# Optimization experiments

Measured on AMD Instinct MI355X. Metric: run time of the kernel, lower is better.

Reference implementation:

```python
import jax, jax.numpy as jnp
import numpy as np

B, L, N = 16, 512, 32          # batch, seq_length, feature_size
E = 128                        # embed_size == frequency_size (number_frequency=1)
EMB = 8                        # embedding_dim
FCH = 64                       # fc_hidden_dim
H = 256                        # hidden_size
PRE = 96                       # pre_length
LAMBDA = 0.01                  # sparsity_threshold
SCALE = 0.02                   # init_scale


def softshrink(v, lambd=LAMBDA):
    return jnp.where(v > lambd, v - lambd, jnp.where(v < -lambd, v + lambd, 0.0))


def setup_inputs() -> dict:
    key = jax.random.key(0)
    ks = jax.random.split(key, 16)
    f32 = jnp.float32
    return {
        "x": jax.random.normal(ks[0], (B, L, N), f32),
        "emb": jax.random.normal(ks[1], (1, E), f32),
        "w0": SCALE * jax.random.normal(ks[2], (2, E, E), f32),
        "b0": SCALE * jax.random.normal(ks[3], (2, E), f32),
        "w1": SCALE * jax.random.normal(ks[4], (2, E, E), f32),
        "b1": SCALE * jax.random.normal(ks[5], (2, E), f32),
        "w2": SCALE * jax.random.normal(ks[6], (2, E, E), f32),
        "b2": SCALE * jax.random.normal(ks[7], (2, E), f32),
        "emb10": jax.random.normal(ks[8], (L, EMB), f32),
        "fc1_w": jax.random.normal(ks[9], (FCH, E * EMB), f32) / np.sqrt(E * EMB),
        "fc1_b": jnp.zeros((FCH,), f32),
        "fc2_w": jax.random.normal(ks[10], (H, FCH), f32) / np.sqrt(FCH),
        "fc2_b": jnp.zeros((H,), f32),
        "fc3_w": jax.random.normal(ks[11], (PRE, H), f32) / np.sqrt(H),
        "fc3_b": jnp.zeros((PRE,), f32),
    }


def _diag(w):
    # einsum 'bli,ii->bli' multiplies by the DIAGONAL of w only
    return jnp.diagonal(w, axis1=-2, axis2=-1)


def reference(x, emb, w0, b0, w1, b1, w2, b2, emb10,
              fc1_w, fc1_b, fc2_w, fc2_b, fc3_w, fc3_b):
    Bb = x.shape[0]
    xt = jnp.transpose(x, (0, 2, 1)).reshape(Bb, -1)          # [B, N*L]
    tok = xt[:, :, None] * emb                                 # [B, N*L, E]
    xf = jnp.fft.rfft(tok, axis=1, norm="ortho")               # [B, N*L//2+1, E] complex
    bias = xf

    # --- fourierGC (faithful to the torch op ordering, incl. o_real reuse) ---
    relu = jax.nn.relu
    d00, d01 = _diag(w0[0]), _diag(w0[1])
    o_r = relu(xf.real * d00 - xf.imag * d01 + b0[0])
    o_i = relu(xf.imag * d00 + xf.real * d01 + b0[1])
    prev = softshrink(jnp.stack([o_r, o_i], axis=-1))

    # middle layer (num_layers=3 -> one): note o_i uses the UPDATED o_r, as in torch
    d10, d11 = _diag(w1[0]), _diag(w1[1])
    o_r_new = relu(o_r * d10 - o_i * d11 + b1[0])
    o_i = relu(o_i * d10 + o_r_new * d11 + b1[1])
    o_r = o_r_new
    prev = softshrink(jnp.stack([o_r, o_i], axis=-1)) + prev

    # last layer
    d20, d21 = _diag(w2[0]), _diag(w2[1])
    o_r_new = relu(o_r * d20 - o_i * d21 + b2[0])
    o_i = relu(o_i * d20 + o_r_new * d21 + b2[1])
    z = softshrink(jnp.stack([o_r_new, o_i], axis=-1)) + prev
    zc = jax.lax.complex(z[..., 0], z[..., 1])

    xf = zc + bias
    xt = jnp.fft.irfft(xf, n=N * L, axis=1, norm="ortho")      # [B, N*L, E]
    xt = xt.reshape(Bb, N, L, E)
    xt = jnp.transpose(xt, (0, 1, 3, 2))                        # [B, N, E, L]
    h = jnp.matmul(xt, emb10)                                   # [B, N, E, EMB]
    h = h.reshape(Bb, N, E * EMB)

    lrelu = lambda v: jax.nn.leaky_relu(v, 0.01)
    h = lrelu(h @ fc1_w.T + fc1_b)
    h = lrelu(h @ fc2_w.T + fc2_b)
    out = h @ fc3_w.T + fc3_b                                   # [B, N, PRE]
    return out[:, 0, :]                                         # target_idx = 0
```

## Files before the change

kernel.cpp:

```cpp
#include <hip/hip_runtime.h>
#include <math.h>

#define Bsz   16
#define Lseq  512
#define Nfeat 32
#define E     128
#define EMB   8
#define FCH   64
#define Hd    256
#define PRE   96
#define M     16384
#define MH    8193
#define LAMBDA 0.01f

#define OFF_G   0
#define OFF_CS  524288
#define OFF_P   655376

#define TWO_PI_M   3.83495196971410293e-4f
#define TWO_PI_128 4.90873852123405245e-2f

__global__ __launch_bounds__(256)
void k_prep(const float* __restrict__ x, const float* __restrict__ emb10,
            float* __restrict__ ws) {
  __shared__ float smem[Lseq * EMB];
  int bid = blockIdx.x, tid = threadIdx.x;
  if (bid < 257) {
    for (int i = tid; i < Lseq * EMB; i += 256) smem[i] = emb10[i];
    __syncthreads();
    int floc = tid >> 5, tl = tid & 31;
    #pragma unroll
    for (int ff = 0; ff < 4; ++ff) {
      int f = bid * 32 + ff * 8 + floc;
      if (f <= 8192) {
        float ca[EMB], sa[EMB];
        #pragma unroll
        for (int m = 0; m < EMB; ++m) { ca[m] = 0.f; sa[m] = 0.f; }
        #pragma unroll 4
        for (int i = 0; i < 16; ++i) {
          int t = tl + 32 * i;
          int k = (f * t) & (M - 1);
          float ss, cc;
          sincosf((float)k * TWO_PI_M, &ss, &cc);
          const float* er = smem + t * EMB;
          #pragma unroll
          for (int m = 0; m < EMB; ++m) {
            ca[m] = fmaf(cc, er[m], ca[m]);
            sa[m] = fmaf(ss, er[m], sa[m]);
          }
        }
        #pragma unroll
        for (int off = 16; off >= 1; off >>= 1) {
          #pragma unroll
          for (int m = 0; m < EMB; ++m) {
            ca[m] += __shfl_xor(ca[m], off, 64);
            sa[m] += __shfl_xor(sa[m], off, 64);
          }
        }
        if (tl == 0) {
          float wf = (f == 0 || f == 8192) ? (1.0f / 128.0f) : (2.0f / 128.0f);
          float* o = ws + OFF_CS + f * 16;
          #pragma unroll
          for (int m = 0; m < EMB; ++m) { o[m] = ca[m] * wf; o[8 + m] = sa[m] * wf; }
        }
      }
    }
  } else {
    int v = bid - 257;
    int b = v >> 6, t1base = (v & 63) << 1;
    int t1loc = tid >> 7, idx = tid & 127;
    {
      int t = (t1base + t1loc) + 128 * idx;
      int n = t >> 9, l = t & 511;
      smem[t1loc * 128 + idx] = x[b * (Lseq * Nfeat) + l * Nfeat + n];
    }
    __syncthreads();
    int f1 = idx, t1 = t1base + t1loc;
    float s1, c1; sincosf((float)f1 * TWO_PI_128, &s1, &c1);
    float c2 = c1 * c1 - s1 * s1, s2 = 2.f * s1 * c1;
    float cA = 1.f, sA = 0.f, cB = c1, sB = s1;
    float grA = 0.f, giA = 0.f, grB = 0.f, giB = 0.f;
    const float* xc = smem + t1loc * 128;
    #pragma unroll 8
    for (int t2 = 0; t2 < 128; t2 += 2) {
      float x0 = xc[t2], x1 = xc[t2 + 1];
      grA = fmaf(x0, cA, grA); giA = fmaf(x0, -sA, giA);
      grB = fmaf(x1, cB, grB); giB = fmaf(x1, -sB, giB);
      float cn = cA * c2 - sA * s2; sA = sA * c2 + cA * s2; cA = cn;
      cn = cB * c2 - sB * s2;       sB = sB * c2 + cB * s2; cB = cn;
    }
    float gr = grA + grB, gi = giA + giB;
    float sb, cb; sincosf((float)(f1 * t1) * TWO_PI_M, &sb, &cb);
    float grr = gr * cb + gi * sb;
    float gii = gi * cb - gr * sb;
    float* G = ws + OFF_G + ((b * 128 + f1) * 128 + t1) * 2;
    G[0] = grr;
    G[1] = gii;
  }
}

__global__ __launch_bounds__(256)
void k_gcf(const float* __restrict__ emb,
           const float* __restrict__ w0, const float* __restrict__ b0,
           const float* __restrict__ w1, const float* __restrict__ b1,
           const float* __restrict__ w2, const float* __restrict__ b2,
           float* __restrict__ ws) {
  int f1 = blockIdx.x, b = blockIdx.y, tid = threadIdx.x;
  int nf2 = (f1 == 0) ? 65 : 64;
  __shared__ float2 Gs[132];
  __shared__ float2 Xs[65];
  __shared__ float red[E * EMB];
  if (tid < 128)
    Gs[(tid >> 5) * 33 + (tid & 31)] =
        ((const float2*)(ws + OFF_G + (b * 128 + f1) * 256))[tid];
  __syncthreads();
  {
    int lane = tid & 63, w = tid >> 6;
    int q = lane >> 4, f2l = lane & 15;
    int f2 = w * 16 + f2l;
    int r = (f2 * q) & 3;
    float c = (r == 0) ? 1.f : (r == 2) ? -1.f : 0.f;
    float s = (r == 1) ? 1.f : (r == 3) ? -1.f : 0.f;
    float s1, c1; sincosf((float)f2 * TWO_PI_128, &s1, &c1);
    float xr = 0.f, xi = 0.f;
    const float2* g = Gs + q * 33;
    #pragma unroll 8
    for (int k = 0; k < 32; ++k) {
      float2 gv = g[k];
      xr = fmaf(gv.x, c, xr); xr = fmaf(gv.y, s, xr);
      xi = fmaf(gv.y, c, xi); xi = fmaf(-gv.x, s, xi);
      float cn = c * c1 - s * s1; s = s * c1 + c * s1; c = cn;
    }
    xr += __shfl_xor(xr, 16, 64); xi += __shfl_xor(xi, 16, 64);
    xr += __shfl_xor(xr, 32, 64); xi += __shfl_xor(xi, 32, 64);
    if (lane < 16) Xs[f2] = make_float2(xr, xi);
    if (f1 == 0 && tid < 32) {
      float er = 0.f, ei = 0.f;
      #pragma unroll
      for (int j = 0; j < 4; ++j) {
        int t1v = tid * 4 + j;
        float2 gv = Gs[(t1v >> 5) * 33 + (t1v & 31)];
        float sg = (j & 1) ? -1.f : 1.f;
        er = fmaf(gv.x, sg, er); ei = fmaf(gv.y, sg, ei);
      }
      #pragma unroll
      for (int off = 1; off <= 16; off <<= 1) {
        er += __shfl_xor(er, off, 64);
        ei += __shfl_xor(ei, off, 64);
      }
      if (tid == 0) Xs[64] = make_float2(er, ei);
    }
  }
  __syncthreads();
  int e = tid & 127, fh = tid >> 7;
  float se  = emb[e] * (1.0f / 128.0f);
  float d00 = w0[e * 129], d01 = w0[E * E + e * 129];
  float c00 = b0[e],       c01 = b0[E + e];
  float d10 = w1[e * 129], d11 = w1[E * E + e * 129];
  float c10 = b1[e],       c11 = b1[E + e];
  float d20 = w2[e * 129], d21 = w2[E * E + e * 129];
  float c20 = b2[e],       c21 = b2[E + e];
  float acc[EMB];
  #pragma unroll
  for (int m = 0; m < EMB; ++m) acc[m] = 0.f;
  const float* csbase = ws + OFF_CS + f1 * 16;

  for (int i = fh; i < nf2; i += 2) {
    int iu = __builtin_amdgcn_readfirstlane(i);
    const float* cs = csbase + (iu << 11);
    float2 X = Xs[i];
    float xr = X.x * se, xi = X.y * se;
    float or0 = fmaxf(fmaf(xr, d00, fmaf(-xi, d01, c00)), 0.f);
    float oi0 = fmaxf(fmaf(xi, d00, fmaf(xr, d01, c01)), 0.f);
    float pr = fmaxf(or0 - LAMBDA, 0.f), pi = fmaxf(oi0 - LAMBDA, 0.f);
    float or1 = fmaxf(fmaf(or0, d10, fmaf(-oi0, d11, c10)), 0.f);
    float oi1 = fmaxf(fmaf(oi0, d10, fmaf(or1, d11, c11)), 0.f);
    pr += fmaxf(or1 - LAMBDA, 0.f); pi += fmaxf(oi1 - LAMBDA, 0.f);
    float u2r = fmaf(or1, d20, fmaf(-oi1, d21, c20));
    float or2 = fmaxf(u2r, 0.f);
    float u2i = fmaf(oi1, d20, fmaf(or2, d21, c21));
    float zr = fmaxf(u2r - LAMBDA, 0.f) + pr;
    float zi = fmaxf(u2i - LAMBDA, 0.f) + pi;
    #pragma unroll
    for (int m = 0; m < EMB; ++m)
      acc[m] = fmaf(zr, cs[m], fmaf(-zi, cs[8 + m], acc[m]));
  }
  __syncthreads();
  if (fh == 1) {
    #pragma unroll
    for (int m = 0; m < EMB; ++m) red[e * EMB + m] = acc[m];
  }
  __syncthreads();
  if (fh == 0) {
    float* P = ws + OFF_P + (f1 * 16 + b) * (E * EMB) + e * EMB;
    #pragma unroll
    for (int m = 0; m < EMB; ++m) P[m] = acc[m] + red[e * EMB + m];
  }
}

__global__ __launch_bounds__(1024)
void k_fc(const float* __restrict__ x, const float* __restrict__ emb,
          const float* __restrict__ emb10,
          const float* __restrict__ fc1w, const float* __restrict__ fc1b,
          const float* __restrict__ fc2w, const float* __restrict__ fc2b,
          const float* __restrict__ fc3w, const float* __restrict__ fc3b,
          const float* __restrict__ ws, float* __restrict__ out) {
  int b = blockIdx.x;
  __shared__ float h0s[E * EMB];
  __shared__ float h1s[FCH];
  __shared__ float h2s[Hd];
  __shared__ float hxs[EMB];
  int tid = threadIdx.x;
  int lane = tid & 63, w = tid >> 6;
  {
    int m = lane & 7, g8 = lane >> 3;
    int gg = w * 8 + g8;
    float p = 0.f;
    #pragma unroll
    for (int l = gg; l < Lseq; l += 128)
      p = fmaf(x[b * (Lseq * Nfeat) + l * Nfeat], emb10[l * EMB + m], p);
    p += __shfl_xor(p, 8, 64);
    p += __shfl_xor(p, 16, 64);
    p += __shfl_xor(p, 32, 64);
    if (lane < 8) h2s[w * 8 + lane] = p;
  }
  const float* P = ws + OFF_P + b * (E * EMB) + tid;
  float a = 0.f;
  #pragma unroll 16
  for (int j = 0; j < 128; ++j) a += P[j * (16 * E * EMB)];
  __syncthreads();
  if (tid < 8) {
    float s = 0.f;
    #pragma unroll
    for (int wv = 0; wv < 16; ++wv) s += h2s[wv * 8 + tid];
    hxs[tid] = s;
  }
  __syncthreads();
  h0s[tid] = a + emb[tid >> 3] * hxs[tid & 7];
  __syncthreads();
  #pragma unroll
  for (int oo = 0; oo < 4; ++oo) {
    int o = oo * 16 + w;
    const float* wr = fc1w + o * (E * EMB);
    float acc = 0.f;
    #pragma unroll
    for (int j = 0; j < 16; ++j) acc = fmaf(h0s[lane + 64 * j], wr[lane + 64 * j], acc);
    #pragma unroll
    for (int off = 32; off >= 1; off >>= 1) acc += __shfl_xor(acc, off, 64);
    if (lane == 0) { float v = acc + fc1b[o]; h1s[o] = v > 0.f ? v : 0.01f * v; }
  }
  __syncthreads();
  #pragma unroll
  for (int oo = 0; oo < 16; ++oo) {
    int o = oo * 16 + w;
    float acc = h1s[lane] * fc2w[o * FCH + lane];
    #pragma unroll
    for (int off = 32; off >= 1; off >>= 1) acc += __shfl_xor(acc, off, 64);
    if (lane == 0) { float v = acc + fc2b[o]; h2s[o] = v > 0.f ? v : 0.01f * v; }
  }
  __syncthreads();
  #pragma unroll
  for (int oo = 0; oo < 6; ++oo) {
    int o = oo * 16 + w;
    const float* wr = fc3w + o * Hd;
    float acc = 0.f;
    #pragma unroll
    for (int j = 0; j < 4; ++j) acc = fmaf(h2s[lane + 64 * j], wr[lane + 64 * j], acc);
    #pragma unroll
    for (int off = 32; off >= 1; off >>= 1) acc += __shfl_xor(acc, off, 64);
    if (lane == 0) out[b * PRE + o] = acc + fc3b[o];
  }
}

extern "C" void kernel_launch(void* const* d_in, const int* in_sizes, int n_in,
                              void* d_out, int out_size, void* d_ws, size_t ws_size,
                              hipStream_t stream) {
  const float* x     = (const float*)d_in[0];
  const float* emb   = (const float*)d_in[1];
  const float* w0    = (const float*)d_in[2];
  const float* b0    = (const float*)d_in[3];
  const float* w1    = (const float*)d_in[4];
  const float* b1    = (const float*)d_in[5];
  const float* w2    = (const float*)d_in[6];
  const float* b2    = (const float*)d_in[7];
  const float* emb10 = (const float*)d_in[8];
  const float* fc1w  = (const float*)d_in[9];
  const float* fc1b  = (const float*)d_in[10];
  const float* fc2w  = (const float*)d_in[11];
  const float* fc2b  = (const float*)d_in[12];
  const float* fc3w  = (const float*)d_in[13];
  const float* fc3b  = (const float*)d_in[14];
  float* ws  = (float*)d_ws;
  float* out = (float*)d_out;

  k_prep<<<dim3(1281), 256, 0, stream>>>(x, emb10, ws);
  k_gcf<<<dim3(128, Bsz), 256, 0, stream>>>(emb, w0, b0, w1, b1, w2, b2, ws);
  k_fc<<<dim3(Bsz), 1024, 0, stream>>>(x, emb, emb10, fc1w, fc1b, fc2w, fc2b,
                                       fc3w, fc3b, ws, out);
}
```

Measured before the change: 153.4 us.

## Merge prep phases, use hardware sin/cos, and batch four f1 rows per gcf block

k_prep now runs both the twiddle-DFT and the cos/sin projection table in every block instead of splitting them across disjoint block ranges. Its sincosf calls become hardware revolution-based sin/cos, and the f=8192 table entry is computed separately. k_gcf handles four f1 rows per block, using a full 128-point inner DFT in place of shuffle-reduced partial sums, which quarters the partial-sum buffer that k_fc must reduce. The intent is fewer launched blocks, cheaper transcendentals and less reduction traffic, at the cost of some hardware sin/cos accuracy and longer per-thread loops.

```diff
diff --git a/kernel.cpp b/kernel.cpp
--- a/kernel.cpp
+++ b/kernel.cpp
@@ -17,142 +17,146 @@
 #define OFF_CS  524288
 #define OFF_P   655376
 
-#define TWO_PI_M   3.83495196971410293e-4f
-#define TWO_PI_128 4.90873852123405245e-2f
-
-__global__ __launch_bounds__(256)
+#define REV_M   6.103515625e-5f
+#define REV_128 7.8125e-3f
+
+__device__ __forceinline__ float sin_rev(float r) { return __builtin_amdgcn_sinf(r); }
+__device__ __forceinline__ float cos_rev(float r) { return __builtin_amdgcn_cosf(r); }
+
+__global__ __launch_bounds__(256, 4)
 void k_prep(const float* __restrict__ x, const float* __restrict__ emb10,
             float* __restrict__ ws) {
-  __shared__ float smem[Lseq * EMB];
+  __shared__ __align__(16) float sbuf[4160];
   int bid = blockIdx.x, tid = threadIdx.x;
-  if (bid < 257) {
-    for (int i = tid; i < Lseq * EMB; i += 256) smem[i] = emb10[i];
-    __syncthreads();
-    int floc = tid >> 5, tl = tid & 31;
-    #pragma unroll
-    for (int ff = 0; ff < 4; ++ff) {
-      int f = bid * 32 + ff * 8 + floc;
-      if (f <= 8192) {
-        float ca[EMB], sa[EMB];
-        #pragma unroll
-        for (int m = 0; m < EMB; ++m) { ca[m] = 0.f; sa[m] = 0.f; }
-        #pragma unroll 4
-        for (int i = 0; i < 16; ++i) {
-          int t = tl + 32 * i;
-          int k = (f * t) & (M - 1);
-          float ss, cc;
-          sincosf((float)k * TWO_PI_M, &ss, &cc);
-          const float* er = smem + t * EMB;
-          #pragma unroll
-          for (int m = 0; m < EMB; ++m) {
-            ca[m] = fmaf(cc, er[m], ca[m]);
-            sa[m] = fmaf(ss, er[m], sa[m]);
-          }
-        }
-        #pragma unroll
-        for (int off = 16; off >= 1; off >>= 1) {
-          #pragma unroll
-          for (int m = 0; m < EMB; ++m) {
-            ca[m] += __shfl_xor(ca[m], off, 64);
-            sa[m] += __shfl_xor(sa[m], off, 64);
-          }
-        }
-        if (tl == 0) {
-          float wf = (f == 0 || f == 8192) ? (1.0f / 128.0f) : (2.0f / 128.0f);
-          float* o = ws + OFF_CS + f * 16;
-          #pragma unroll
-          for (int m = 0; m < EMB; ++m) { o[m] = ca[m] * wf; o[8 + m] = sa[m] * wf; }
-        }
-      }
-    }
-  } else {
-    int v = bid - 257;
-    int b = v >> 6, t1base = (v & 63) << 1;
+  {
+    int b = bid >> 6, t1base = (bid & 63) << 1;
     int t1loc = tid >> 7, idx = tid & 127;
     {
       int t = (t1base + t1loc) + 128 * idx;
       int n = t >> 9, l = t & 511;
-      smem[t1loc * 128 + idx] = x[b * (Lseq * Nfeat) + l * Nfeat + n];
+      sbuf[t1loc * 128 + idx] = x[b * (Lseq * Nfeat) + l * Nfeat + n];
     }
     __syncthreads();
     int f1 = idx, t1 = t1base + t1loc;
-    float s1, c1; sincosf((float)f1 * TWO_PI_128, &s1, &c1);
+    float s1 = sin_rev((float)f1 * REV_128), c1 = cos_rev((float)f1 * REV_128);
     float c2 = c1 * c1 - s1 * s1, s2 = 2.f * s1 * c1;
     float cA = 1.f, sA = 0.f, cB = c1, sB = s1;
     float grA = 0.f, giA = 0.f, grB = 0.f, giB = 0.f;
-    const float* xc = smem + t1loc * 128;
+    const float2* xc2 = (const float2*)(sbuf + t1loc * 128);
     #pragma unroll 8
-    for (int t2 = 0; t2 < 128; t2 += 2) {
-      float x0 = xc[t2], x1 = xc[t2 + 1];
-      grA = fmaf(x0, cA, grA); giA = fmaf(x0, -sA, giA);
-      grB = fmaf(x1, cB, grB); giB = fmaf(x1, -sB, giB);
+    for (int h = 0; h < 64; ++h) {
+      float2 xv = xc2[h];
+      grA = fmaf(xv.x, cA, grA); giA = fmaf(xv.x, -sA, giA);
+      grB = fmaf(xv.y, cB, grB); giB = fmaf(xv.y, -sB, giB);
       float cn = cA * c2 - sA * s2; sA = sA * c2 + cA * s2; cA = cn;
       cn = cB * c2 - sB * s2;       sB = sB * c2 + cB * s2; cB = cn;
     }
     float gr = grA + grB, gi = giA + giB;
-    float sb, cb; sincosf((float)(f1 * t1) * TWO_PI_M, &sb, &cb);
+    float rv = (float)(f1 * t1) * REV_M;
+    float sb = sin_rev(rv), cb = cos_rev(rv);
     float grr = gr * cb + gi * sb;
     float gii = gi * cb - gr * sb;
     float* G = ws + OFF_G + ((b * 128 + f1) * 128 + t1) * 2;
-    G[0] = grr;
-    G[1] = gii;
+    G[0] = grr; G[1] = gii;
+  }
+  __syncthreads();
+  {
+    for (int j = tid; j < Lseq * EMB; j += 256) {
+      int t = j >> 3, m = j & 7;
+      sbuf[m * 512 + t] = emb10[j];
+    }
+    __syncthreads();
+    int floc = tid >> 5, tl = tid & 31;
+    int f = bid * 8 + floc;
+    float ca[EMB], sa[EMB];
+    #pragma unroll
+    for (int m = 0; m < EMB; ++m) { ca[m] = 0.f; sa[m] = 0.f; }
+    #pragma unroll 4
+    for (int it = 0; it < 16; ++it) {
+      int t = tl + 32 * it;
+      int k = (f * t) & (M - 1);
+      float rv = (float)k * REV_M;
+      float cc = cos_rev(rv), ss = sin_rev(rv);
+      #pragma unroll
+      for (int m = 0; m < EMB; ++m) {
+        float ev = sbuf[m * 512 + t];
+        ca[m] = fmaf(cc, ev, ca[m]);
+        sa[m] = fmaf(ss, ev, sa[m]);
+      }
+    }
+    #pragma unroll
+    for (int off = 16; off >= 1; off >>= 1) {
+      #pragma unroll
+      for (int m = 0; m < EMB; ++m) {
+        ca[m] += __shfl_xor(ca[m], off, 64);
+        sa[m] += __shfl_xor(sa[m], off, 64);
+      }
+    }
+    if (tl == 0) {
+      float wf = (f == 0) ? (1.0f / 128.0f) : (2.0f / 128.0f);
+      float* o = ws + OFF_CS + f * 16;
+      #pragma unroll
+      for (int m = 0; m < EMB; ++m) { o[m] = ca[m] * wf; o[8 + m] = sa[m] * wf; }
+    }
+    if (bid == 0 && tid < 64) {
+      int m = tid & 7, g = tid >> 3;
+      float p = 0.f;
+      #pragma unroll 8
+      for (int j = 0; j < 64; ++j) p += sbuf[m * 512 + g + 8 * j];
+      p = (g & 1) ? -p : p;
+      p += __shfl_xor(p, 8, 64);
+      p += __shfl_xor(p, 16, 64);
+      p += __shfl_xor(p, 32, 64);
+      if (g == 0) {
+        ws[OFF_CS + 8192 * 16 + m] = p * (1.0f / 128.0f);
+        ws[OFF_CS + 8192 * 16 + 8 + m] = 0.f;
+      }
+    }
   }
 }
 
-__global__ __launch_bounds__(256)
+__global__ __launch_bounds__(256, 4)
 void k_gcf(const float* __restrict__ emb,
            const float* __restrict__ w0, const float* __restrict__ b0,
            const float* __restrict__ w1, const float* __restrict__ b1,
            const float* __restrict__ w2, const float* __restrict__ b2,
            float* __restrict__ ws) {
-  int f1 = blockIdx.x, b = blockIdx.y, tid = threadIdx.x;
-  int nf2 = (f1 == 0) ? 65 : 64;
-  __shared__ float2 Gs[132];
-  __shared__ float2 Xs[65];
+  __shared__ __align__(16) float2 Gs[4][128];
+  __shared__ __align__(16) float2 Xs[257];
   __shared__ float red[E * EMB];
-  if (tid < 128)
-    Gs[(tid >> 5) * 33 + (tid & 31)] =
-        ((const float2*)(ws + OFF_G + (b * 128 + f1) * 256))[tid];
+  int f1g = blockIdx.x, b = blockIdx.y, tid = threadIdx.x;
+  int f1base = f1g * 4;
+  ((float4*)Gs)[tid] =
+      ((const float4*)(ws + OFF_G + (b * 128 + f1base) * 256))[tid];
   __syncthreads();
   {
-    int lane = tid & 63, w = tid >> 6;
-    int q = lane >> 4, f2l = lane & 15;
-    int f2 = w * 16 + f2l;
-    int r = (f2 * q) & 3;
-    float c = (r == 0) ? 1.f : (r == 2) ? -1.f : 0.f;
-    float s = (r == 1) ? 1.f : (r == 3) ? -1.f : 0.f;
-    float s1, c1; sincosf((float)f2 * TWO_PI_128, &s1, &c1);
+    int f1loc = tid >> 6, f2 = tid & 63;
+    float s1 = sin_rev((float)f2 * REV_128), c1 = cos_rev((float)f2 * REV_128);
+    float c = 1.f, s = 0.f;
     float xr = 0.f, xi = 0.f;
-    const float2* g = Gs + q * 33;
+    const float2* g = Gs[f1loc];
     #pragma unroll 8
-    for (int k = 0; k < 32; ++k) {
-      float2 gv = g[k];
+    for (int t1 = 0; t1 < 128; ++t1) {
+      float2 gv = g[t1];
       xr = fmaf(gv.x, c, xr); xr = fmaf(gv.y, s, xr);
       xi = fmaf(gv.y, c, xi); xi = fmaf(-gv.x, s, xi);
       float cn = c * c1 - s * s1; s = s * c1 + c * s1; c = cn;
     }
-    xr += __shfl_xor(xr, 16, 64); xi += __shfl_xor(xi, 16, 64);
-    xr += __shfl_xor(xr, 32, 64); xi += __shfl_xor(xi, 32, 64);
-    if (lane < 16) Xs[f2] = make_float2(xr, xi);
-    if (f1 == 0 && tid < 32) {
-      float er = 0.f, ei = 0.f;
+    Xs[f1loc * 64 + f2] = make_float2(xr, xi);
+    if (f1base == 0 && tid < 64) {
+      float2 g0 = Gs[0][tid * 2], g1 = Gs[0][tid * 2 + 1];
+      float er = g0.x - g1.x, ei = g0.y - g1.y;
       #pragma unroll
-      for (int j = 0; j < 4; ++j) {
-        int t1v = tid * 4 + j;
-        float2 gv = Gs[(t1v >> 5) * 33 + (t1v & 31)];
-        float sg = (j & 1) ? -1.f : 1.f;
-        er = fmaf(gv.x, sg, er); ei = fmaf(gv.y, sg, ei);
-      }
-      #pragma unroll
-      for (int off = 1; off <= 16; off <<= 1) {
+      for (int off = 1; off <= 32; off <<= 1) {
         er += __shfl_xor(er, off, 64);
         ei += __shfl_xor(ei, off, 64);
       }
-      if (tid == 0) Xs[64] = make_float2(er, ei);
+      if (tid == 0) Xs[256] = make_float2(er, ei);
     }
   }
   __syncthreads();
   int e = tid & 127, fh = tid >> 7;
+  int nf = (f1base == 0) ? 257 : 256;
   float se  = emb[e] * (1.0f / 128.0f);
   float d00 = w0[e * 129], d01 = w0[E * E + e * 129];
   float c00 = b0[e],       c01 = b0[E + e];
@@ -163,12 +167,12 @@
   float acc[EMB];
   #pragma unroll
   for (int m = 0; m < EMB; ++m) acc[m] = 0.f;
-  const float* csbase = ws + OFF_CS + f1 * 16;
-
-  for (int i = fh; i < nf2; i += 2) {
+
+  for (int i = fh; i < nf; i += 2) {
     int iu = __builtin_amdgcn_readfirstlane(i);
-    const float* cs = csbase + (iu << 11);
-    float2 X = Xs[i];
+    int f = (iu == 256) ? 8192 : (f1base + (iu >> 6) + ((iu & 63) << 7));
+    const float* cs = ws + OFF_CS + f * 16;
+    float2 X = Xs[iu];
     float xr = X.x * se, xi = X.y * se;
     float or0 = fmaxf(fmaf(xr, d00, fmaf(-xi, d01, c00)), 0.f);
     float oi0 = fmaxf(fmaf(xi, d00, fmaf(xr, d01, c01)), 0.f);
@@ -192,7 +196,7 @@
   }
   __syncthreads();
   if (fh == 0) {
-    float* P = ws + OFF_P + (f1 * 16 + b) * (E * EMB) + e * EMB;
+    float* P = ws + OFF_P + (f1g * 16 + b) * (E * EMB) + e * EMB;
     #pragma unroll
     for (int m = 0; m < EMB; ++m) P[m] = acc[m] + red[e * EMB + m];
   }
@@ -210,29 +214,26 @@
   __shared__ float h1s[FCH];
   __shared__ float h2s[Hd];
   __shared__ float hxs[EMB];
+  __shared__ float scratch[1024];
   int tid = threadIdx.x;
   int lane = tid & 63, w = tid >> 6;
   {
-    int m = lane & 7, g8 = lane >> 3;
-    int gg = w * 8 + g8;
+    int m = tid & 7, g = tid >> 3;
     float p = 0.f;
     #pragma unroll
-    for (int l = gg; l < Lseq; l += 128)
+    for (int l = g; l < Lseq; l += 128)
       p = fmaf(x[b * (Lseq * Nfeat) + l * Nfeat], emb10[l * EMB + m], p);
-    p += __shfl_xor(p, 8, 64);
-    p += __shfl_xor(p, 16, 64);
-    p += __shfl_xor(p, 32, 64);
-    if (lane < 8) h2s[w * 8 + lane] = p;
+    scratch[tid] = p;
   }
   const float* P = ws + OFF_P + b * (E * EMB) + tid;
   float a = 0.f;
-  #pragma unroll 16
-  for (int j = 0; j < 128; ++j) a += P[j * (16 * E * EMB)];
+  #pragma unroll
+  for (int c = 0; c < 32; ++c) a += P[c * (Bsz * E * EMB)];
   __syncthreads();
   if (tid < 8) {
     float s = 0.f;
-    #pragma unroll
-    for (int wv = 0; wv < 16; ++wv) s += h2s[wv * 8 + tid];
+    #pragma unroll 16
+    for (int g = 0; g < 128; ++g) s += scratch[g * 8 + tid];
     hxs[tid] = s;
   }
   __syncthreads();
@@ -293,8 +294,8 @@
   float* ws  = (float*)d_ws;
   float* out = (float*)d_out;
 
-  k_prep<<<dim3(1281), 256, 0, stream>>>(x, emb10, ws);
-  k_gcf<<<dim3(128, Bsz), 256, 0, stream>>>(emb, w0, b0, w1, b1, w2, b2, ws);
+  k_prep<<<dim3(1024), 256, 0, stream>>>(x, emb10, ws);
+  k_gcf<<<dim3(32, Bsz), 256, 0, stream>>>(emb, w0, b0, w1, b1, w2, b2, ws);
   k_fc<<<dim3(Bsz), 1024, 0, stream>>>(x, emb, emb10, fc1w, fc1b, fc2w, fc2b,
                                        fc3w, fc3b, ws, out);
 }
```

New measurement: 177.1 us. 15.4% more time.
